# Optimization experiments

Measured on AMD Instinct MI355X. Metric: run time of the kernel, lower is better.

## Reference

```python
import jax, jax.numpy as jnp
import numpy as np

EPSILON = 0.1      # init kwarg epsilon
NUM_STAB = 1e-06   # init kwarg num_stab
B, D, C = 4096, 3072, 10


def setup_inputs() -> dict:
    key = jax.random.key(0)
    k1, k2 = jax.random.split(key)
    data = jax.random.normal(k1, (B, D), dtype=jnp.float32)
    # small scale keeps softmax probs near-uniform -> rho well-conditioned
    W = jax.random.normal(k2, (D, C), dtype=jnp.float32) * 0.02
    return {"data": data, "W": W}


def _probs(logits, c):
    # output = softmax(...) * (1 - c*num_stab) + num_stab  (numerical stabilization)
    p = jax.nn.softmax(logits, axis=-1)
    return p * (1.0 - c * NUM_STAB) + NUM_STAB


def reference(data, W):
    c = W.shape[1]
    m = c - 1

    def g(x):  # x: [D] -> new_output row: [m]
        p = _probs(x @ W, c)
        s = jnp.sqrt(p)
        return 2.0 * s[:m] / (1.0 - s[m])

    # Vectorized Jacobian: replaces the m sequential autograd.grad calls.
    jac = jax.vmap(jax.jacrev(g))(data)            # [B, m, D]

    p = _probs(data @ W, c)                        # [B, C]
    s_m = jnp.sqrt(p[:, m])                        # [B]
    delta = 2.0 * jnp.arccos(jnp.sqrt(p / c).sum(axis=1))   # [B]
    rho = (2.0 * (1.0 - s_m) - p[:, :m].sum(axis=1)) / (1.0 - s_m)  # [B]
    jac_norm = jnp.sqrt(jnp.square(jac).sum(axis=(1, 2)))   # [B] Frobenius norm per sample
    reg = jax.nn.elu(jac_norm - delta / (rho * EPSILON))
    return reg.mean()
```

## Files before the change

### kernel.cpp

```cpp
#include <hip/hip_runtime.h>
#include <math.h>

#define NB 4096
#define ND 3072
#define NC 10
#define NM 9

static constexpr float kEps      = 0.1f;
static constexpr float kNumStab  = 1e-6f;
static constexpr float kAlpha    = 1.0f - (float)NC * kNumStab;
static constexpr float kInvSqrtC = 0.31622776601683794f;

__global__ void gram_kernel(const float* __restrict__ W, float* __restrict__ G) {
    const int j = blockIdx.x / NC;
    const int k = blockIdx.x % NC;
    float acc = 0.0f;
    for (int d = threadIdx.x; d < ND; d += 256) {
        acc += W[d * NC + j] * W[d * NC + k];
    }
    #pragma unroll
    for (int off = 32; off > 0; off >>= 1) acc += __shfl_xor(acc, off, 64);
    __shared__ float part[4];
    const int lane = threadIdx.x & 63;
    const int wv   = threadIdx.x >> 6;
    if (lane == 0) part[wv] = acc;
    __syncthreads();
    if (threadIdx.x == 0) G[blockIdx.x] = part[0] + part[1] + part[2] + part[3];
}

__global__ __launch_bounds__(512) void jacreg_kernel(
        const float* __restrict__ data, const float* __restrict__ W,
        const float* __restrict__ G, float* __restrict__ out) {
    __shared__ float Wts[NC * ND];
    __shared__ float Gs[100];
    __shared__ float regs[16];

    const int tid  = threadIdx.x;
    const int lane = tid & 63;
    const int wv   = tid >> 6;

    if (tid < 100) Gs[tid] = G[tid];

    for (int i = tid; i < (ND * NC) / 4; i += 512) {
        const float4 w4 = reinterpret_cast<const float4*>(W)[i];
        const float* wp = reinterpret_cast<const float*>(&w4);
        const int e0 = i * 4;
        #pragma unroll
        for (int j = 0; j < 4; ++j) {
            const int e = e0 + j;
            Wts[(e % NC) * ND + (e / NC)] = wp[j];
        }
    }
    __syncthreads();

    const int s0 = blockIdx.x * 16 + wv * 2;
    const float* __restrict__ r0 = data + (size_t)s0 * ND;
    const float* __restrict__ r1 = r0 + ND;

    float acc[2][NC];
    #pragma unroll
    for (int s = 0; s < 2; ++s)
        #pragma unroll
        for (int k = 0; k < NC; ++k) acc[s][k] = 0.0f;

    float4 x0 = reinterpret_cast<const float4*>(r0)[lane];
    float4 x1 = reinterpret_cast<const float4*>(r1)[lane];
    for (int it = 0; it < 12; ++it) {
        const int nit = (it == 11) ? 11 : it + 1;
        const float4 nx0 = reinterpret_cast<const float4*>(r0)[nit * 64 + lane];
        const float4 nx1 = reinterpret_cast<const float4*>(r1)[nit * 64 + lane];

        const int dbase = it * 256 + lane * 4;
        #pragma unroll
        for (int k = 0; k < NC; ++k) {
            const float4 wt = *reinterpret_cast<const float4*>(&Wts[k * ND + dbase]);
            acc[0][k] = fmaf(x0.x, wt.x, acc[0][k]);
            acc[0][k] = fmaf(x0.y, wt.y, acc[0][k]);
            acc[0][k] = fmaf(x0.z, wt.z, acc[0][k]);
            acc[0][k] = fmaf(x0.w, wt.w, acc[0][k]);
            acc[1][k] = fmaf(x1.x, wt.x, acc[1][k]);
            acc[1][k] = fmaf(x1.y, wt.y, acc[1][k]);
            acc[1][k] = fmaf(x1.z, wt.z, acc[1][k]);
            acc[1][k] = fmaf(x1.w, wt.w, acc[1][k]);
        }
        x0 = nx0;
        x1 = nx1;
    }

    #pragma unroll
    for (int s = 0; s < 2; ++s)
        #pragma unroll
        for (int k = 0; k < NC; ++k) {
            float v = acc[s][k];
            #pragma unroll
            for (int off = 32; off > 0; off >>= 1) v += __shfl_xor(v, off, 64);
            acc[s][k] = v;
        }

    if (lane < 2) {
        float z[NC];
        #pragma unroll
        for (int k = 0; k < NC; ++k) z[k] = (lane == 0) ? acc[0][k] : acc[1][k];

        float zm = z[0];
        #pragma unroll
        for (int k = 1; k < NC; ++k) zm = fmaxf(zm, z[k]);
        float e[NC], Zs = 0.0f;
        #pragma unroll
        for (int k = 0; k < NC; ++k) { e[k] = expf(z[k] - zm); Zs += e[k]; }
        const float inv = 1.0f / Zs;

        float sg[NC], p[NC], sq[NC], u[NC];
        #pragma unroll
        for (int k = 0; k < NC; ++k) {
            sg[k] = e[k] * inv;
            p[k]  = kAlpha * sg[k] + kNumStab;
            sq[k] = sqrtf(p[k]);
            u[k]  = sg[k] / sq[k];
        }
        const float q = 1.0f - sq[NM];

        float v[NC], t = 0.0f;
        #pragma unroll
        for (int k = 0; k < NC; ++k) {
            float a = 0.0f;
            #pragma unroll
            for (int j = 0; j < NC; ++j) a = fmaf(Gs[k * NC + j], sg[j], a);
            v[k] = a;
            t = fmaf(sg[k], a, t);
        }
        const float vM = v[NM], uM = u[NM];
        const float QMM = Gs[NC * NC - 1] - 2.0f * vM + t;

        float sumJ = 0.0f;
        #pragma unroll
        for (int i = 0; i < NM; ++i) {
            const float Qii = Gs[i * NC + i] - 2.0f * v[i] + t;
            const float QiM = Gs[i * NC + NM] - v[i] - vM + t;
            const float r = sq[i] / q;
            sumJ += u[i] * u[i] * Qii
                  + 2.0f * u[i] * uM * r * QiM
                  + uM * uM * r * r * QMM;
        }
        const float jn = (kAlpha / q) * sqrtf(fmaxf(sumJ, 0.0f));

        float ssum = 0.0f;
        #pragma unroll
        for (int k = 0; k < NC; ++k) ssum += sq[k];
        const float ac = fminf(1.0f, fmaxf(-1.0f, ssum * kInvSqrtC));
        const float delta = 2.0f * acosf(ac);

        float psum = 0.0f;
        #pragma unroll
        for (int k = 0; k < NM; ++k) psum += p[k];
        const float rho = (2.0f * q - psum) / q;

        const float a = jn - delta / (rho * kEps);
        regs[wv * 2 + lane] = (a > 0.0f) ? a : expm1f(a);
    }
    __syncthreads();
    if (tid == 0) {
        float bs = 0.0f;
        #pragma unroll
        for (int i = 0; i < 16; ++i) bs += regs[i];
        atomicAdd(out, bs * (1.0f / (float)NB));
    }
}

extern "C" void kernel_launch(void* const* d_in, const int* in_sizes, int n_in,
                              void* d_out, int out_size, void* d_ws, size_t ws_size,
                              hipStream_t stream) {
    const float* data = (const float*)d_in[0];
    const float* W    = (const float*)d_in[1];
    float* out = (float*)d_out;
    float* G   = (float*)d_ws;

    hipMemsetAsync(out, 0, sizeof(float), stream);
    gram_kernel<<<NC * NC, 256, 0, stream>>>(W, G);
    jacreg_kernel<<<NB / 16, 512, 0, stream>>>(data, W, G, out);
}
```

Baseline: 98.51 us.

## Fold output zeroing into single-block Gram kernel and deepen data prefetch

Replaces the 100-block Gram kernel and the separate memset with one 1024-thread block. That block computes the 55 unique symmetric Gram entries from W staged in LDS and also zeroes the output, which removes one launch. The main kernel now issues its first data-row loads before the W transpose into LDS, and it prefetches two iterations ahead instead of one, to hide global-load latency. The cost is more registers per thread in the main kernel, and the Gram work now runs serially on a single CU.

```diff
diff --git a/kernel.cpp b/kernel.cpp
--- a/kernel.cpp
+++ b/kernel.cpp
@@ -11,21 +11,67 @@
 static constexpr float kAlpha    = 1.0f - (float)NC * kNumStab;
 static constexpr float kInvSqrtC = 0.31622776601683794f;
 
-__global__ void gram_kernel(const float* __restrict__ W, float* __restrict__ G) {
-    const int j = blockIdx.x / NC;
-    const int k = blockIdx.x % NC;
-    float acc = 0.0f;
-    for (int d = threadIdx.x; d < ND; d += 256) {
-        acc += W[d * NC + j] * W[d * NC + k];
-    }
-    #pragma unroll
-    for (int off = 32; off > 0; off >>= 1) acc += __shfl_xor(acc, off, 64);
-    __shared__ float part[4];
-    const int lane = threadIdx.x & 63;
-    const int wv   = threadIdx.x >> 6;
-    if (lane == 0) part[wv] = acc;
-    __syncthreads();
-    if (threadIdx.x == 0) G[blockIdx.x] = part[0] + part[1] + part[2] + part[3];
+__global__ __launch_bounds__(1024) void gram_zero_kernel(
+        const float* __restrict__ W, float* __restrict__ G,
+        float* __restrict__ out) {
+    __shared__ float Wls[ND * NC];
+    __shared__ float part[16][56];
+
+    const int tid  = threadIdx.x;
+    const int lane = tid & 63;
+    const int wv   = tid >> 6;
+
+    for (int i = tid; i < (ND * NC) / 4; i += 1024) {
+        reinterpret_cast<float4*>(Wls)[i] = reinterpret_cast<const float4*>(W)[i];
+    }
+    __syncthreads();
+
+    float a[55];
+    #pragma unroll
+    for (int c = 0; c < 55; ++c) a[c] = 0.0f;
+
+    #pragma unroll
+    for (int rr = 0; rr < 3; ++rr) {
+        const int row = tid + rr * 1024;
+        const float* rp = &Wls[row * NC];
+        float r[NC];
+        #pragma unroll
+        for (int h = 0; h < 5; ++h) {
+            const float2 v = *reinterpret_cast<const float2*>(rp + 2 * h);
+            r[2 * h] = v.x; r[2 * h + 1] = v.y;
+        }
+        int c = 0;
+        #pragma unroll
+        for (int i = 0; i < NC; ++i)
+            #pragma unroll
+            for (int j = i; j < NC; ++j) {
+                a[c] = fmaf(r[i], r[j], a[c]);
+                ++c;
+            }
+    }
+
+    #pragma unroll
+    for (int c = 0; c < 55; ++c) {
+        #pragma unroll
+        for (int off = 32; off > 0; off >>= 1) a[c] += __shfl_xor(a[c], off, 64);
+    }
+    if (lane == 0) {
+        #pragma unroll
+        for (int c = 0; c < 55; ++c) part[wv][c] = a[c];
+    }
+    __syncthreads();
+
+    if (tid < 55) {
+        float g = 0.0f;
+        #pragma unroll
+        for (int w = 0; w < 16; ++w) g += part[w][tid];
+        int idx = tid, i = 0;
+        while (idx >= (NC - i)) { idx -= (NC - i); ++i; }
+        const int j = i + idx;
+        G[i * NC + j] = g;
+        G[j * NC + i] = g;
+    }
+    if (tid == 1023) out[0] = 0.0f;
 }
 
 __global__ __launch_bounds__(512) void jacreg_kernel(
@@ -39,6 +85,15 @@
     const int lane = tid & 63;
     const int wv   = tid >> 6;
 
+    const int s0 = blockIdx.x * 16 + wv * 2;
+    const float* __restrict__ r0 = data + (size_t)s0 * ND;
+    const float* __restrict__ r1 = r0 + ND;
+
+    float4 x0a = reinterpret_cast<const float4*>(r0)[lane];
+    float4 x1a = reinterpret_cast<const float4*>(r1)[lane];
+    float4 x0b = reinterpret_cast<const float4*>(r0)[64 + lane];
+    float4 x1b = reinterpret_cast<const float4*>(r1)[64 + lane];
+
     if (tid < 100) Gs[tid] = G[tid];
 
     for (int i = tid; i < (ND * NC) / 4; i += 512) {
@@ -53,38 +108,32 @@
     }
     __syncthreads();
 
-    const int s0 = blockIdx.x * 16 + wv * 2;
-    const float* __restrict__ r0 = data + (size_t)s0 * ND;
-    const float* __restrict__ r1 = r0 + ND;
-
     float acc[2][NC];
     #pragma unroll
     for (int s = 0; s < 2; ++s)
         #pragma unroll
         for (int k = 0; k < NC; ++k) acc[s][k] = 0.0f;
 
-    float4 x0 = reinterpret_cast<const float4*>(r0)[lane];
-    float4 x1 = reinterpret_cast<const float4*>(r1)[lane];
     for (int it = 0; it < 12; ++it) {
-        const int nit = (it == 11) ? 11 : it + 1;
-        const float4 nx0 = reinterpret_cast<const float4*>(r0)[nit * 64 + lane];
-        const float4 nx1 = reinterpret_cast<const float4*>(r1)[nit * 64 + lane];
+        const int pit = (it + 2 <= 11) ? it + 2 : 11;
+        const float4 n0 = reinterpret_cast<const float4*>(r0)[pit * 64 + lane];
+        const float4 n1 = reinterpret_cast<const float4*>(r1)[pit * 64 + lane];
 
         const int dbase = it * 256 + lane * 4;
         #pragma unroll
         for (int k = 0; k < NC; ++k) {
             const float4 wt = *reinterpret_cast<const float4*>(&Wts[k * ND + dbase]);
-            acc[0][k] = fmaf(x0.x, wt.x, acc[0][k]);
-            acc[0][k] = fmaf(x0.y, wt.y, acc[0][k]);
-            acc[0][k] = fmaf(x0.z, wt.z, acc[0][k]);
-            acc[0][k] = fmaf(x0.w, wt.w, acc[0][k]);
-            acc[1][k] = fmaf(x1.x, wt.x, acc[1][k]);
-            acc[1][k] = fmaf(x1.y, wt.y, acc[1][k]);
-            acc[1][k] = fmaf(x1.z, wt.z, acc[1][k]);
-            acc[1][k] = fmaf(x1.w, wt.w, acc[1][k]);
-        }
-        x0 = nx0;
-        x1 = nx1;
+            acc[0][k] = fmaf(x0a.x, wt.x, acc[0][k]);
+            acc[0][k] = fmaf(x0a.y, wt.y, acc[0][k]);
+            acc[0][k] = fmaf(x0a.z, wt.z, acc[0][k]);
+            acc[0][k] = fmaf(x0a.w, wt.w, acc[0][k]);
+            acc[1][k] = fmaf(x1a.x, wt.x, acc[1][k]);
+            acc[1][k] = fmaf(x1a.y, wt.y, acc[1][k]);
+            acc[1][k] = fmaf(x1a.z, wt.z, acc[1][k]);
+            acc[1][k] = fmaf(x1a.w, wt.w, acc[1][k]);
+        }
+        x0a = x0b; x1a = x1b;
+        x0b = n0;  x1b = n1;
     }
 
     #pragma unroll
@@ -175,7 +224,6 @@
     float* out = (float*)d_out;
     float* G   = (float*)d_ws;
 
-    hipMemsetAsync(out, 0, sizeof(float), stream);
-    gram_kernel<<<NC * NC, 256, 0, stream>>>(W, G);
+    gram_zero_kernel<<<1, 1024, 0, stream>>>(W, G, out);
     jacreg_kernel<<<NB / 16, 512, 0, stream>>>(data, W, G, out);
 }
```

Measured after the change: 110.4 us. 1.12x slower.
